# Performance work log

Measured on AMD Instinct MI355X. Metric: run time of the kernel, lower is better.

## Reference

```python
import jax, jax.numpy as jnp
import numpy as np
from jax.ops import segment_sum, segment_max

N, H, E, NEXP, K, L, HEADS, NM = 384, 768, 12288, 8, 2, 3, 4, 38
GAMMA, LAMBDA_SPD = 2.0, 0.5


def _ln(x, g, b, eps=1e-5):
    m = jnp.mean(x, -1, keepdims=True)
    v = jnp.mean((x - m) ** 2, -1, keepdims=True)
    return (x - m) / jnp.sqrt(v + eps) * g + b


def _gelu(x):
    return jax.nn.gelu(x, approximate=False)


def setup_inputs() -> dict:
    key = jax.random.key(0)
    ks = jax.random.split(key, 20)
    r = lambda i, sh: jax.random.normal(ks[i], sh, jnp.float32) * 0.02
    z = lambda sh: jnp.zeros(sh, jnp.float32)
    o = lambda sh: jnp.ones(sh, jnp.float32)
    return dict(
        feat_text=jax.random.normal(ks[0], (N, H), jnp.float32),
        feat_image=jax.random.normal(ks[1], (N, H), jnp.float32),
        spd_matrix=jax.random.uniform(ks[2], (N, N), dtype=jnp.float32),
        src=jax.random.randint(ks[3], (E,), 0, N, jnp.int32),
        dst=jax.random.randint(ks[4], (E,), 0, N, jnp.int32),
        mask_idx=jax.random.randint(ks[5], (NM,), 0, N, jnp.int32),
        mask_token=r(6, (H,)),
        gate_W=r(7, (H, NEXP)), gate_b=z((NEXP,)),
        exp_W1=r(8, (NEXP, H, H)), exp_b1=z((NEXP, H)),
        exp_g1=o((NEXP, H)), exp_be1=z((NEXP, H)),
        exp_W2=r(9, (NEXP, H, H)), exp_b2=z((NEXP, H)),
        gat_W=r(10, (L, H, HEADS * H)), gat_al=r(11, (L, HEADS, H)),
        gat_ar=r(12, (L, HEADS, H)), gat_b=z((L, HEADS * H)),
        dec_W1=r(13, (2, H, H)), dec_b1=z((2, H)),
        dec_g=o((2, H)), dec_be=z((2, H)),
        dec_W2=r(14, (2, H, H)), dec_b2=z((2, H)),
        spd_W1=r(15, (2 * H, H)), spd_b1=z((H,)),
        spd_g=o((H,)), spd_be=z((H,)),
        spd_W2=r(16, (H, 1)), spd_b2=z((1,)),
    )


def _forward(feat_text, feat_image, spd_matrix, mask_token, gate_W, gate_b,
             exp_W1, exp_b1, exp_g1, exp_be1, exp_W2, exp_b2,
             gat_W, gat_al, gat_ar, gat_b,
             dec_W1, dec_b1, dec_g, dec_be, dec_W2, dec_b2,
             spd_W1, spd_b1, spd_g, spd_be, spd_W2, spd_b2,
             src, dst, mask_idx):
    # mean of domain features, then mask-token replacement at fixed indices
    x = (feat_text + feat_image) * 0.5
    xm = x.at[mask_idx].set(mask_token)

    # --- MoE (all experts computed densely, top-2 gathered, as in source) ---
    gw = jax.nn.softmax(xm @ gate_W + gate_b, axis=-1)              # [N,NEXP]
    topw, topi = jax.lax.top_k(gw, K)
    topw = topw / jnp.sum(topw, -1, keepdims=True)
    eh = _gelu(_ln(jnp.einsum('nd,edh->neh', xm, exp_W1) + exp_b1, exp_g1, exp_be1))
    eo = jnp.einsum('neh,ehk->nek', eh, exp_W2) + exp_b2            # [N,NEXP,H]
    sel = jnp.take_along_axis(eo, topi[:, :, None], axis=1)          # [N,K,H]
    h = jnp.sum(sel * topw[:, :, None], axis=1)                      # [N,H]

    # --- stacked GATConv layers (DGL semantics), head-mean after each ---
    for l in range(L):
        f = (h @ gat_W[l]).reshape(N, HEADS, H)                      # [N,heads,H]
        el = jnp.sum(f * gat_al[l], -1)                              # [N,heads]
        er = jnp.sum(f * gat_ar[l], -1)
        e = jax.nn.leaky_relu(el[src] + er[dst], 0.2)                # [E,heads]
        emax = segment_max(e, dst, num_segments=N)
        emax = jnp.where(jnp.isfinite(emax), emax, 0.0)
        ex = jnp.exp(e - emax[dst])
        den = segment_sum(ex, dst, num_segments=N)
        alpha = ex / jnp.maximum(den[dst], 1e-9)                     # edge softmax by dst
        rst = segment_sum(alpha[:, :, None] * f[src], dst, num_segments=N)
        h = jnp.mean(rst + gat_b[l].reshape(HEADS, H), axis=1)       # [N,H]

    # --- domain reconstruction loss on masked nodes ---
    hm = h[mask_idx]
    feats = (feat_text, feat_image)
    recon = jnp.float32(0.0)
    for d in range(2):
        zz = _gelu(_ln(hm @ dec_W1[d] + dec_b1[d], dec_g[d], dec_be[d]))
        rec = zz @ dec_W2[d] + dec_b2[d]
        orig = feats[d][mask_idx]
        denom = jnp.maximum(jnp.linalg.norm(rec, axis=-1) * jnp.linalg.norm(orig, axis=-1), 1e-8)
        cos = jnp.sum(rec * orig, -1) / denom
        recon = recon + jnp.mean((1.0 - cos) ** GAMMA)

    # --- SPD loss over all N^2 pairs, vectorized ---
    # concat([h_i, h_j]) @ W1 == h_i @ W1[:H] + h_j @ W1[H:]  (exact decomposition)
    pa = h @ spd_W1[:H]                                              # [N,H]
    pb = h @ spd_W1[H:]                                              # [N,H]
    zp = _gelu(_ln(pa[:, None, :] + pb[None, :, :] + spd_b1, spd_g, spd_be))  # [N,N,H]
    pred = (zp @ spd_W2)[..., 0] + spd_b2[0]                         # [N,N]
    spd_loss = jnp.mean((pred - spd_matrix) ** 2)

    total = recon + LAMBDA_SPD * spd_loss
    return total, h


def reference(feat_text, feat_image, spd_matrix, src, dst, mask_idx, mask_token,
              gate_W, gate_b, exp_W1, exp_b1, exp_g1, exp_be1, exp_W2, exp_b2,
              gat_W, gat_al, gat_ar, gat_b,
              dec_W1, dec_b1, dec_g, dec_be, dec_W2, dec_b2,
              spd_W1, spd_b1, spd_g, spd_be, spd_W2, spd_b2):
    return _forward(feat_text, feat_image, spd_matrix, mask_token, gate_W, gate_b,
                    exp_W1, exp_b1, exp_g1, exp_be1, exp_W2, exp_b2,
                    gat_W, gat_al, gat_ar, gat_b,
                    dec_W1, dec_b1, dec_g, dec_be, dec_W2, dec_b2,
                    spd_W1, spd_b1, spd_g, spd_be, spd_W2, spd_b2,
                    src, dst, mask_idx)
```

## Files before the change

kernel.cpp:

```cpp
#include <hip/hip_runtime.h>
#include <hip/hip_bf16.h>
#include <math.h>

#define NN 384
#define HD 768
#define EE 12288
#define NCHUNK (EE / 256)
#define NEXPERT 8
#define TOPK 2
#define NLAYER 3
#define NHEADS 4
#define NMASK 38

typedef __attribute__((ext_vector_type(8))) short short8v;
typedef __attribute__((ext_vector_type(4))) float f32x4;
typedef __attribute__((ext_vector_type(2))) float f32x2;
typedef __attribute__((ext_vector_type(4))) int int4v;

__device__ __forceinline__ float gelu_f(float x) {
    return x * 0.5f * (1.f + erff(x * 0.70710678118654752440f));
}

__device__ __forceinline__ ushort f2bf(float x) {
    unsigned u = __float_as_uint(x);
    u += 0x7fffu + ((u >> 16) & 1u);
    return (ushort)(u >> 16);
}

__global__ __launch_bounds__(256) void k_xm_gate_hist(const float* __restrict__ a,
        const float* __restrict__ b, const int* __restrict__ mask_idx,
        const float* __restrict__ mt, ushort* __restrict__ xm_bf,
        const float* __restrict__ gW, const float* __restrict__ gb,
        int* __restrict__ topi, float* __restrict__ topw,
        const int* __restrict__ dst, int* __restrict__ counts) {
    if (blockIdx.x >= NN) {
        __shared__ int h[NN];
        int c = blockIdx.x - NN;
        for (int i = threadIdx.x; i < NN; i += 256) h[i] = 0;
        __syncthreads();
        atomicAdd(&h[dst[c * 256 + threadIdx.x]], 1);
        __syncthreads();
        for (int i = threadIdx.x; i < NN; i += 256) counts[c * NN + i] = h[i];
        return;
    }
    int n = blockIdx.x, tid = threadIdx.x;
    __shared__ float xs[HD];
    __shared__ int ism;
    __shared__ float logits[NEXPERT];
    if (tid == 0) ism = 0;
    __syncthreads();
    if (tid < NMASK && mask_idx[tid] == n) ism = 1;
    __syncthreads();
#pragma unroll
    for (int r = 0; r < 3; r++) {
        int j = r * 256 + tid;
        float v = ism ? mt[j] : 0.5f * (a[(size_t)n * HD + j] + b[(size_t)n * HD + j]);
        xs[j] = v;
        xm_bf[(size_t)n * HD + j] = f2bf(v);
    }
    __syncthreads();
    int grp = tid >> 5;
    int l32 = tid & 31;
    float p = 0.f;
    for (int dd = l32; dd < HD; dd += 32) p += xs[dd] * gW[dd * NEXPERT + grp];
#pragma unroll
    for (int m = 1; m < 32; m <<= 1) p += __shfl_xor(p, m, 32);
    if (l32 == 0) logits[grp] = p + gb[grp];
    __syncthreads();
    if (tid == 0) {
        float mx = logits[0];
#pragma unroll
        for (int e = 1; e < NEXPERT; e++) mx = fmaxf(mx, logits[e]);
        float sm[NEXPERT]; float s = 0.f;
#pragma unroll
        for (int e = 0; e < NEXPERT; e++) { sm[e] = expf(logits[e] - mx); s += sm[e]; }
#pragma unroll
        for (int e = 0; e < NEXPERT; e++) sm[e] /= s;
        int i0 = 0; float b0 = sm[0];
#pragma unroll
        for (int e = 1; e < NEXPERT; e++) if (sm[e] > b0) { b0 = sm[e]; i0 = e; }
        int i1 = -1; float b1v = -1.f;
#pragma unroll
        for (int e = 0; e < NEXPERT; e++) if (e != i0 && sm[e] > b1v) { b1v = sm[e]; i1 = e; }
        float ssum = b0 + b1v;
        topi[n * 2] = i0; topi[n * 2 + 1] = i1;
        topw[n * 2] = b0 / ssum; topw[n * 2 + 1] = b1v / ssum;
    }
}

__global__ __launch_bounds__(256) void k_transpose_all(
        const float* __restrict__ w1, const float* __restrict__ w2,
        const float* __restrict__ gw, const float* __restrict__ sw,
        const float* __restrict__ dw1, const float* __restrict__ dw2,
        ushort* __restrict__ o1, ushort* __restrict__ o2, ushort* __restrict__ og,
        ushort* __restrict__ os, ushort* __restrict__ od1, ushort* __restrict__ od2) {
    int b = blockIdx.x;
    const float* src; ushort* dst; int N, loc, tilesX;
    if (b < 2304)      { src = w1;  dst = o1;  N = HD;     loc = b;        tilesX = 24; }
    else if (b < 4608) { src = w2;  dst = o2;  N = HD;     loc = b - 2304; tilesX = 24; }
    else if (b < 8064) { src = gw;  dst = og;  N = 4 * HD; loc = b - 4608; tilesX = 96; }
    else if (b < 8640) { src = sw;  dst = os;  N = HD;     loc = b - 8064; tilesX = 24; }
    else if (b < 9216) { src = dw1; dst = od1; N = HD;     loc = b - 8640; tilesX = 24; }
    else               { src = dw2; dst = od2; N = HD;     loc = b - 9216; tilesX = 24; }
    const int K = HD;
    int tilesPerZ = tilesX * 12;
    int z = loc / tilesPerZ;
    int rem = loc - z * tilesPerZ;
    int ty = rem / tilesX, tx = rem - ty * tilesX;
    const float* inz = src + (size_t)z * K * N;
    ushort* outz = dst + (size_t)z * K * N;
    int n0 = tx * 32, k0 = ty * 64;

    __shared__ float t[64][33];
    int r = threadIdx.x >> 2, c8 = (threadIdx.x & 3) * 8;
    const float* ip = inz + (size_t)(k0 + r) * N + n0 + c8;
    float4 va = *reinterpret_cast<const float4*>(ip);
    float4 vb = *reinterpret_cast<const float4*>(ip + 4);
    t[r][c8 + 0] = va.x; t[r][c8 + 1] = va.y; t[r][c8 + 2] = va.z; t[r][c8 + 3] = va.w;
    t[r][c8 + 4] = vb.x; t[r][c8 + 5] = vb.y; t[r][c8 + 6] = vb.z; t[r][c8 + 7] = vb.w;
    __syncthreads();
    int nn = threadIdx.x >> 3;
    int kk = (threadIdx.x & 7) * 8;
    uint4 o;
    uint pk[4];
#pragma unroll
    for (int q = 0; q < 4; q++) {
        ushort lo = f2bf(t[kk + 2 * q][nn]);
        ushort hi = f2bf(t[kk + 2 * q + 1][nn]);
        pk[q] = (uint)lo | ((uint)hi << 16);
    }
    o.x = pk[0]; o.y = pk[1]; o.z = pk[2]; o.w = pk[3];
    *reinterpret_cast<uint4*>(outz + (size_t)(n0 + nn) * K + k0 + kk) = o;
}

__global__ __launch_bounds__(NN) void k_scan_meta(const int* __restrict__ counts,
        int* __restrict__ chunkbase, int* __restrict__ nstart,
        const int* __restrict__ topi, int* __restrict__ ecnt, int* __restrict__ estart,
        int* __restrict__ posArr, int* __restrict__ eofpos, int* __restrict__ rowlist,
        int* __restrict__ dec_rs) {
    int tid = threadIdx.x;
    if (blockIdx.x == 0) {
        __shared__ int tot[NN];
        int n = tid;
        int s = 0;
        for (int c = 0; c < NCHUNK; c++) { chunkbase[c * NN + n] = s; s += counts[c * NN + n]; }
        tot[n] = s;
        __syncthreads();
        for (int off = 1; off < NN; off <<= 1) {
            int v = tot[n];
            int add = (n >= off) ? tot[n - off] : 0;
            __syncthreads();
            tot[n] = v + add;
            __syncthreads();
        }
        nstart[n + 1] = tot[n];
        if (n == 0) nstart[0] = 0;
        return;
    }
    __shared__ int ti[NN * TOPK];
    __shared__ int cnt[NEXPERT];
    __shared__ int est[NEXPERT + 1];
    if (tid < NEXPERT) cnt[tid] = 0;
    __syncthreads();
    for (int a = tid; a < NN * TOPK; a += NN) ti[a] = topi[a];
    __syncthreads();
    for (int a = tid; a < NN * TOPK; a += NN) atomicAdd(&cnt[ti[a]], 1);
    __syncthreads();
    if (tid == 0) {
        int s = 0;
        for (int e = 0; e < NEXPERT; e++) { est[e] = s; s += cnt[e]; }
        est[NEXPERT] = s;
        dec_rs[0] = 0; dec_rs[1] = NMASK;
    }
    __syncthreads();
    if (tid < NEXPERT) { ecnt[tid] = cnt[tid]; estart[tid] = est[tid]; }
    if (tid == 0) estart[NEXPERT] = est[NEXPERT];
    for (int a = tid; a < NN * TOPK; a += NN) {
        int e = ti[a]; int rank = 0;
        for (int a2 = 0; a2 < a; a2++) rank += (ti[a2] == e) ? 1 : 0;
        int p = est[e] + rank;
        posArr[a] = p; eofpos[p] = e; rowlist[p] = a >> 1;
    }
}

__global__ __launch_bounds__(256) void k_rank2(const int* __restrict__ dst,
        const int* __restrict__ chunkbase, const int* __restrict__ nstart,
        int* __restrict__ esorted) {
    __shared__ int ds[256];
    int c = blockIdx.x;
    int e = c * 256 + threadIdx.x;
    int d = dst[e];
    ds[threadIdx.x] = d;
    __syncthreads();
    int r = 0;
    for (int i = 0; i < threadIdx.x; i++) r += (ds[i] == d) ? 1 : 0;
    esorted[nstart[d] + chunkbase[c * NN + d] + r] = e;
}

__device__ __forceinline__ short8v ldfrag(const ushort* s, int r, int kb) {
    int c = kb ^ (r & 7);
    return *reinterpret_cast<const short8v*>(s + r * 64 + c * 8);
}

__device__ __forceinline__ void gemm_body(
        const ushort* __restrict__ A, const ushort* __restrict__ Bt, float* __restrict__ C,
        int M, int Ncol, int K, int lda, int ldc, long strideBt, long strideC,
        const int* __restrict__ rowsA, const int* __restrict__ Ms,
        const int* __restrict__ rowStarts, int z, ushort* Asm, ushort* Bsm) {
    int Meff = Ms ? Ms[z] : M;
    int row0 = blockIdx.y * 64;
    if (row0 >= Meff) return;
    int col0 = blockIdx.x * 64;
    if (col0 >= Ncol) return;
    int rowbase = rowStarts ? rowStarts[z] : 0;
    const ushort* Btz = Bt + (size_t)z * strideBt;
    float* Cz = C + (size_t)rowbase * ldc + (size_t)z * strideC;
    const int* rz = rowsA ? (rowsA + rowbase) : nullptr;

    int tid = threadIdx.x;
    int w = tid >> 6, lane = tid & 63;
    int wr = w >> 1, wc = w & 1;
    int l15 = lane & 15, lq = lane >> 4;

    int r0s = tid >> 3, c0s = tid & 7;
    int cs0 = c0s ^ (r0s & 7);
    int r1s = r0s + 32;
    int cs1 = c0s ^ (r1s & 7);
    int grow0 = row0 + r0s, grow1 = row0 + r1s;
    bool ok0 = grow0 < Meff, ok1 = grow1 < Meff;
    int srow0 = ok0 ? (rz ? rz[grow0] : rowbase + grow0) : (rz ? rz[0] : rowbase);
    int srow1 = ok1 ? (rz ? rz[grow1] : rowbase + grow1) : (rz ? rz[0] : rowbase);
    const ushort* aP0 = A + (size_t)srow0 * lda + c0s * 8;
    const ushort* aP1 = A + (size_t)srow1 * lda + c0s * 8;
    const ushort* bP0 = Btz + (size_t)(col0 + r0s) * K + c0s * 8;
    const ushort* bP1 = Btz + (size_t)(col0 + r1s) * K + c0s * 8;
    ushort* asm0 = &Asm[r0s * 64 + cs0 * 8];
    ushort* asm1 = &Asm[r1s * 64 + cs1 * 8];
    ushort* bsm0 = &Bsm[r0s * 64 + cs0 * 8];
    ushort* bsm1 = &Bsm[r1s * 64 + cs1 * 8];
    const int4v z4 = (int4v){0, 0, 0, 0};

    f32x4 acc[2][2];
#pragma unroll
    for (int i = 0; i < 2; i++)
#pragma unroll
        for (int j = 0; j < 2; j++) acc[i][j] = (f32x4){0.f, 0.f, 0.f, 0.f};

    int4v ta0 = *reinterpret_cast<const int4v*>(aP0);
    int4v ta1 = *reinterpret_cast<const int4v*>(aP1);
    int4v av0 = ok0 ? ta0 : z4;
    int4v av1 = ok1 ? ta1 : z4;
    int4v bv0 = *reinterpret_cast<const int4v*>(bP0);
    int4v bv1 = *reinterpret_cast<const int4v*>(bP1);

    for (int k0 = 0; k0 < K; k0 += 64) {
        *reinterpret_cast<int4v*>(asm0) = av0;
        *reinterpret_cast<int4v*>(asm1) = av1;
        *reinterpret_cast<int4v*>(bsm0) = bv0;
        *reinterpret_cast<int4v*>(bsm1) = bv1;
        __syncthreads();
        int kn = k0 + 64;
        if (kn < K) {
            int4v na0 = *reinterpret_cast<const int4v*>(aP0 + kn);
            int4v na1 = *reinterpret_cast<const int4v*>(aP1 + kn);
            av0 = ok0 ? na0 : z4;
            av1 = ok1 ? na1 : z4;
            bv0 = *reinterpret_cast<const int4v*>(bP0 + kn);
            bv1 = *reinterpret_cast<const int4v*>(bP1 + kn);
        }
#pragma unroll
        for (int ks = 0; ks < 2; ks++) {
            int kb = ks * 4 + lq;
            short8v a0 = ldfrag(Asm, wr * 32 + l15, kb);
            short8v a1 = ldfrag(Asm, wr * 32 + 16 + l15, kb);
            short8v b0 = ldfrag(Bsm, wc * 32 + l15, kb);
            short8v b1 = ldfrag(Bsm, wc * 32 + 16 + l15, kb);
            acc[0][0] = __builtin_amdgcn_mfma_f32_16x16x32_bf16(a0, b0, acc[0][0], 0, 0, 0);
            acc[0][1] = __builtin_amdgcn_mfma_f32_16x16x32_bf16(a0, b1, acc[0][1], 0, 0, 0);
            acc[1][0] = __builtin_amdgcn_mfma_f32_16x16x32_bf16(a1, b0, acc[1][0], 0, 0, 0);
            acc[1][1] = __builtin_amdgcn_mfma_f32_16x16x32_bf16(a1, b1, acc[1][1], 0, 0, 0);
        }
        __syncthreads();
    }
#pragma unroll
    for (int ai = 0; ai < 2; ai++)
#pragma unroll
        for (int bi = 0; bi < 2; bi++) {
            int rbase = row0 + wr * 32 + ai * 16 + (lq << 2);
            int cc = col0 + wc * 32 + bi * 16 + l15;
#pragma unroll
            for (int r = 0; r < 4; r++) {
                int rr = rbase + r;
                if (rr < Meff) Cz[(size_t)rr * ldc + cc] = acc[ai][bi][r];
            }
        }
}

__global__ __launch_bounds__(256) void k_mfma_gemm(
        const ushort* __restrict__ A, const ushort* __restrict__ Bt, float* __restrict__ C,
        int M, int Ncol, int K, int lda, int ldc, long strideBt, long strideC,
        const int* __restrict__ rowsA, const int* __restrict__ Ms,
        const int* __restrict__ rowStarts) {
    __shared__ ushort Asm[64 * 64];
    __shared__ ushort Bsm[64 * 64];
    gemm_body(A, Bt, C, M, Ncol, K, lda, ldc, strideBt, strideC, rowsA, Ms, rowStarts,
              blockIdx.z, Asm, Bsm);
}

__global__ __launch_bounds__(256) void k_mfma_dual(
        const ushort* __restrict__ A0, const ushort* __restrict__ Bt0, float* __restrict__ C0,
        int M0, int Nc0, int lda0, int ldc0, long sBt0, long sC0,
        const int* __restrict__ rows0, const int* __restrict__ rs0, int nz0,
        const ushort* __restrict__ A1, const ushort* __restrict__ Bt1, float* __restrict__ C1,
        int M1, int Nc1, int lda1, int ldc1, long sBt1, long sC1,
        const int* __restrict__ rows1, const int* __restrict__ rs1) {
    __shared__ ushort Asm[64 * 64];
    __shared__ ushort Bsm[64 * 64];
    int z = blockIdx.z;
    if (z < nz0)
        gemm_body(A0, Bt0, C0, M0, Nc0, HD, lda0, ldc0, sBt0, sC0, rows0, nullptr, rs0,
                  z, Asm, Bsm);
    else
        gemm_body(A1, Bt1, C1, M1, Nc1, HD, lda1, ldc1, sBt1, sC1, rows1, nullptr, rs1,
                  z - nz0, Asm, Bsm);
}

__global__ __launch_bounds__(256) void k_ln_gelu(const float* __restrict__ t1,
        ushort* __restrict__ ehb, const float* __restrict__ b1, const float* __restrict__ g,
        const float* __restrict__ be, const int* __restrict__ eofpos) {
    int row = blockIdx.x;
    int e = eofpos[row];
    int tid = threadIdx.x;
    __shared__ float rA[4], rB[4];
    float v[3]; float s1 = 0.f, s2 = 0.f;
#pragma unroll
    for (int r = 0; r < 3; r++) {
        int c = r * 256 + tid;
        float x = t1[(size_t)row * HD + c] + b1[e * HD + c];
        v[r] = x; s1 += x; s2 += x * x;
    }
#pragma unroll
    for (int m = 1; m < 64; m <<= 1) { s1 += __shfl_xor(s1, m); s2 += __shfl_xor(s2, m); }
    int wave = tid >> 6, lane = tid & 63;
    if (lane == 0) { rA[wave] = s1; rB[wave] = s2; }
    __syncthreads();
    float S1 = rA[0] + rA[1] + rA[2] + rA[3];
    float S2 = rB[0] + rB[1] + rB[2] + rB[3];
    float mean = S1 * (1.f / HD);
    float var = S2 * (1.f / HD) - mean * mean;
    float rstd = rsqrtf(var + 1e-5f);
#pragma unroll
    for (int r = 0; r < 3; r++) {
        int c = r * 256 + tid;
        float zn = (v[r] - mean) * rstd * g[e * HD + c] + be[e * HD + c];
        ehb[(size_t)row * HD + c] = f2bf(gelu_f(zn));
    }
}

__global__ void k_combine_moe(const float* __restrict__ eo, const float* __restrict__ b2,
        const int* __restrict__ topi, const float* __restrict__ topw,
        const int* __restrict__ posArr, float* __restrict__ h, ushort* __restrict__ hb) {
    int n = blockIdx.x;
    int tid = threadIdx.x;
    int e0 = topi[n * 2], e1 = topi[n * 2 + 1];
    float w0 = topw[n * 2], w1 = topw[n * 2 + 1];
    int p0 = posArr[n * 2], p1 = posArr[n * 2 + 1];
    for (int j = tid; j < HD; j += 256) {
        float v0 = eo[(size_t)p0 * HD + j] + b2[e0 * HD + j];
        float v1 = eo[(size_t)p1 * HD + j] + b2[e1 * HD + j];
        float hv = w0 * v0 + w1 * v1;
        h[(size_t)n * HD + j] = hv;
        hb[(size_t)n * HD + j] = f2bf(hv);
    }
}

__global__ __launch_bounds__(256) void k_el_er(const float* __restrict__ f,
        const float* __restrict__ al, const float* __restrict__ ar,
        float* __restrict__ el, float* __restrict__ er) {
    int n = blockIdx.x;
    int hd = threadIdx.x >> 6, lane = threadIdx.x & 63;
    const float* fr = f + ((size_t)n * NHEADS + hd) * HD;
    float pl = 0.f, pr = 0.f;
    for (int j = lane; j < HD; j += 64) {
        float fv = fr[j];
        pl += fv * al[hd * HD + j];
        pr += fv * ar[hd * HD + j];
    }
#pragma unroll
    for (int m = 1; m < 64; m <<= 1) { pl += __shfl_xor(pl, m); pr += __shfl_xor(pr, m); }
    if (lane == 0) { el[n * NHEADS + hd] = pl; er[n * NHEADS + hd] = pr; }
}

__global__ __launch_bounds__(256) void k_gat_agg(const float* __restrict__ f,
        const float* __restrict__ el, const float* __restrict__ er,
        const int* __restrict__ src, const int* __restrict__ esorted,
        const int* __restrict__ nstart, const float* __restrict__ gb,
        float* __restrict__ hout, ushort* __restrict__ hb, float* __restrict__ outp) {
    int n = blockIdx.x;
    int s0 = nstart[n], cnt = nstart[n + 1] - s0;
    int tid = threadIdx.x;
    __shared__ float red[4][NHEADS];
    __shared__ float emax_s[NHEADS], den_s[NHEADS];
    __shared__ float alpha_s[256][NHEADS];
    __shared__ int sn_s[256];
    float ern[NHEADS];
#pragma unroll
    for (int hd = 0; hd < NHEADS; hd++) ern[hd] = er[n * NHEADS + hd];
    int wave = tid >> 6, lane = tid & 63;

    float mx[NHEADS] = { -1e30f, -1e30f, -1e30f, -1e30f };
    for (int t = tid; t < cnt; t += 256) {
        int e = esorted[s0 + t]; int sn = src[e];
#pragma unroll
        for (int hd = 0; hd < NHEADS; hd++) {
            float v = el[sn * NHEADS + hd] + ern[hd];
            v = (v >= 0.f) ? v : 0.2f * v;
            mx[hd] = fmaxf(mx[hd], v);
        }
    }
#pragma unroll
    for (int hd = 0; hd < NHEADS; hd++) {
#pragma unroll
        for (int m = 1; m < 64; m <<= 1) mx[hd] = fmaxf(mx[hd], __shfl_xor(mx[hd], m));
    }
    if (lane == 0) { for (int hd = 0; hd < NHEADS; hd++) red[wave][hd] = mx[hd]; }
    __syncthreads();
    if (tid == 0) {
#pragma unroll
        for (int hd = 0; hd < NHEADS; hd++)
            emax_s[hd] = fmaxf(fmaxf(red[0][hd], red[1][hd]), fmaxf(red[2][hd], red[3][hd]));
    }
    __syncthreads();
    float sm[NHEADS] = { 0.f, 0.f, 0.f, 0.f };
    for (int t = tid; t < cnt; t += 256) {
        int e = esorted[s0 + t]; int sn = src[e];
#pragma unroll
        for (int hd = 0; hd < NHEADS; hd++) {
            float v = el[sn * NHEADS + hd] + ern[hd];
            v = (v >= 0.f) ? v : 0.2f * v;
            sm[hd] += expf(v - emax_s[hd]);
        }
    }
#pragma unroll
    for (int hd = 0; hd < NHEADS; hd++) {
#pragma unroll
        for (int m = 1; m < 64; m <<= 1) sm[hd] += __shfl_xor(sm[hd], m);
    }
    __syncthreads();
    if (lane == 0) { for (int hd = 0; hd < NHEADS; hd++) red[wave][hd] = sm[hd]; }
    __syncthreads();
    if (tid == 0) {
#pragma unroll
        for (int hd = 0; hd < NHEADS; hd++)
            den_s[hd] = red[0][hd] + red[1][hd] + red[2][hd] + red[3][hd];
    }
    __syncthreads();
    float acc[NHEADS][3] = {};
    for (int c0 = 0; c0 < cnt; c0 += 256) {
        int t = c0 + tid;
        if (t < cnt) {
            int e = esorted[s0 + t]; int sn = src[e];
            sn_s[tid] = sn;
#pragma unroll
            for (int hd = 0; hd < NHEADS; hd++) {
                float v = el[sn * NHEADS + hd] + ern[hd];
                v = (v >= 0.f) ? v : 0.2f * v;
                alpha_s[tid][hd] = expf(v - emax_s[hd]) / fmaxf(den_s[hd], 1e-9f);
            }
        }
        __syncthreads();
        int cm = cnt - c0; if (cm > 256) cm = 256;
        for (int i = 0; i < cm; i++) {
            int sn = sn_s[i];
            const float* fr = f + (size_t)sn * (NHEADS * HD);
#pragma unroll
            for (int hd = 0; hd < NHEADS; hd++) {
                float a = alpha_s[i][hd];
#pragma unroll
                for (int r = 0; r < 3; r++) acc[hd][r] += a * fr[hd * HD + r * 256 + tid];
            }
        }
        __syncthreads();
    }
#pragma unroll
    for (int r = 0; r < 3; r++) {
        int j = r * 256 + tid;
        float s = 0.f;
#pragma unroll
        for (int hd = 0; hd < NHEADS; hd++) s += acc[hd][r] + gb[hd * HD + j];
        float hv = 0.25f * s;
        hout[(size_t)n * HD + j] = hv;
        hb[(size_t)n * HD + j] = f2bf(hv);
        if (outp) outp[1 + (size_t)n * HD + j] = hv;
    }
}

__global__ __launch_bounds__(256) void k_lndec_prep(float* __restrict__ pab,
        const float* __restrict__ b1, ushort* __restrict__ pp_bf,
        float* __restrict__ Svec, float* __restrict__ Qvec,
        const float* __restrict__ t1, ushort* __restrict__ zzb,
        const float* __restrict__ db1, const float* __restrict__ dg,
        const float* __restrict__ dbe) {
    int tid = threadIdx.x;
    int wave = tid >> 6, lane = tid & 63;
    __shared__ float rA[4], rB[4];
    if (blockIdx.x >= 2 * NN) {
        int row = blockIdx.x - 2 * NN;
        int d = row / NMASK;
        float v[3]; float s1 = 0.f, s2 = 0.f;
#pragma unroll
        for (int r = 0; r < 3; r++) {
            int c = r * 256 + tid;
            float x = t1[(size_t)row * HD + c] + db1[d * HD + c];
            v[r] = x; s1 += x; s2 += x * x;
        }
#pragma unroll
        for (int mm = 1; mm < 64; mm <<= 1) { s1 += __shfl_xor(s1, mm); s2 += __shfl_xor(s2, mm); }
        if (lane == 0) { rA[wave] = s1; rB[wave] = s2; }
        __syncthreads();
        float S1 = rA[0] + rA[1] + rA[2] + rA[3];
        float S2 = rB[0] + rB[1] + rB[2] + rB[3];
        float mean = S1 * (1.f / HD);
        float var = S2 * (1.f / HD) - mean * mean;
        float rstd = rsqrtf(var + 1e-5f);
#pragma unroll
        for (int r = 0; r < 3; r++) {
            int c = r * 256 + tid;
            float zn = (v[r] - mean) * rstd * dg[d * HD + c] + dbe[d * HD + c];
            zzb[(size_t)row * HD + c] = f2bf(gelu_f(zn));
        }
        return;
    }
    int r = blockIdx.x;
    bool isA = r < NN;
    float* row = pab + (size_t)r * HD;
    float vv[3]; float s1 = 0.f, s2 = 0.f;
#pragma unroll
    for (int rr = 0; rr < 3; rr++) {
        int j = rr * 256 + tid;
        float v = row[j];
        if (isA) v += b1[j];
        vv[rr] = v; s1 += v; s2 += v * v;
    }
#pragma unroll
    for (int m = 1; m < 64; m <<= 1) { s1 += __shfl_xor(s1, m); s2 += __shfl_xor(s2, m); }
    if (lane == 0) { rA[wave] = s1; rB[wave] = s2; }
#pragma unroll
    for (int rr = 0; rr < 3; rr++) {
        int j = rr * 256 + tid;
        if (isA) row[j] = vv[rr];
        pp_bf[(size_t)r * HD + j] = f2bf(vv[rr]);
    }
    __syncthreads();
    if (tid == 0) {
        Svec[r] = rA[0] + rA[1] + rA[2] + rA[3];
        Qvec[r] = rB[0] + rB[1] + rB[2] + rB[3];
    }
}

#define GC1 2.3022085f
#define GC2 0.10294429f
__global__ __launch_bounds__(256) void k_spd2(const float* __restrict__ pab,
        const float* __restrict__ Svec, const float* __restrict__ Qvec,
        const float* __restrict__ cross, const float* __restrict__ g,
        const float* __restrict__ be, const float* __restrict__ w2,
        const float* __restrict__ b2, const float* __restrict__ spd,
        float* __restrict__ partials,
        const float* __restrict__ rec, const float* __restrict__ db2,
        const int* __restrict__ mask_idx, const float* __restrict__ ft,
        const float* __restrict__ fi, float* __restrict__ rec_part) {
    int wv = threadIdx.x >> 6, lane = threadIdx.x & 63;
    if (blockIdx.y == 8) {
        int b = blockIdx.x;
        if (b >= 2 * NMASK) return;
        int d = b / NMASK, m = b % NMASK;
        int node = mask_idx[m];
        int tid = threadIdx.x;
        __shared__ float rA[4], rB[4], rC[4];
        const float* rrow = rec + (size_t)b * HD;
        const float* orig = (d == 0 ? ft : fi) + (size_t)node * HD;
        float pro = 0.f, prr = 0.f, poo = 0.f;
#pragma unroll
        for (int r = 0; r < 3; r++) {
            int c = r * 256 + tid;
            float rv = rrow[c] + db2[d * HD + c];
            float o = orig[c];
            pro += rv * o; prr += rv * rv; poo += o * o;
        }
#pragma unroll
        for (int mm = 1; mm < 64; mm <<= 1) {
            pro += __shfl_xor(pro, mm); prr += __shfl_xor(prr, mm); poo += __shfl_xor(poo, mm);
        }
        if (lane == 0) { rA[wv] = pro; rB[wv] = prr; rC[wv] = poo; }
        __syncthreads();
        if (tid == 0) {
            float P = rA[0] + rA[1] + rA[2] + rA[3];
            float R = rB[0] + rB[1] + rB[2] + rB[3];
            float O = rC[0] + rC[1] + rC[2] + rC[3];
            float denom = fmaxf(sqrtf(R) * sqrtf(O), 1e-8f);
            float cosv = P / denom;
            float t = 1.f - cosv;
            rec_part[b] = (t * t) * (1.f / (float)NMASK);
        }
        return;
    }
    int i = blockIdx.x;
    int y = blockIdx.y * 4 + wv;
    const f32x2* paP = reinterpret_cast<const f32x2*>(pab + (size_t)i * HD) + lane;
    const f32x2* gP  = reinterpret_cast<const f32x2*>(g) + lane;
    const f32x2* beP = reinterpret_cast<const f32x2*>(be) + lane;
    const f32x2* wP  = reinterpret_cast<const f32x2*>(w2) + lane;
    f32x2 pa2[6], g2[6], be2[6], w22[6];
#pragma unroll
    for (int s = 0; s < 6; s++) {
        pa2[s] = paP[s * 64];
        g2[s]  = gP[s * 64];
        be2[s] = beP[s * 64];
        w22[s] = wP[s * 64];
    }
#pragma unroll
    for (int s = 0; s < 6; s++) {
        asm volatile("" : "+v"(pa2[s]), "+v"(g2[s]), "+v"(be2[s]), "+v"(w22[s]));
    }
    const f32x2 C1v = (f32x2){GC1, GC1};
    const f32x2 C2v = (f32x2){GC2, GC2};
    const f32x2 one2 = (f32x2){1.f, 1.f};
    float Sa = Svec[i], Qa = Qvec[i];
    float b2v = b2[0];
    float bacc = 0.f;
#pragma unroll
    for (int t = 0; t < 6; t++) {
        int ja = y + (2 * t) * 32;
        int jb = y + (2 * t + 1) * 32;
        const f32x2* pA = reinterpret_cast<const f32x2*>(pab + (size_t)(NN + ja) * HD) + lane;
        const f32x2* pB = reinterpret_cast<const f32x2*>(pab + (size_t)(NN + jb) * HD) + lane;
        float meanA = (Sa + Svec[NN + ja]) * (1.f / HD);
        float exA = (Qa + Qvec[NN + ja] + 2.f * cross[(size_t)i * NN + ja]) * (1.f / HD);
        float rsA = rsqrtf(exA - meanA * meanA + 1e-5f);
        float nmA = -meanA * rsA;
        float meanB = (Sa + Svec[NN + jb]) * (1.f / HD);
        float exB = (Qa + Qvec[NN + jb] + 2.f * cross[(size_t)i * NN + jb]) * (1.f / HD);
        float rsB = rsqrtf(exB - meanB * meanB + 1e-5f);
        float nmB = -meanB * rsB;
        f32x2 rsA2 = (f32x2){rsA, rsA}, nmA2 = (f32x2){nmA, nmA};
        f32x2 rsB2 = (f32x2){rsB, rsB}, nmB2 = (f32x2){nmB, nmB};
        f32x2 dA = (f32x2){0.f, 0.f}, dB = (f32x2){0.f, 0.f};
#pragma unroll
        for (int s = 0; s < 6; s++) {
            f32x2 zA = pa2[s] + pA[s * 64];
            f32x2 zB = pa2[s] + pB[s * 64];
            f32x2 znA = (zA * rsA2 + nmA2) * g2[s] + be2[s];
            f32x2 znB = (zB * rsB2 + nmB2) * g2[s] + be2[s];
            f32x2 uaA = znA * (znA * znA * C2v + C1v);
            f32x2 uaB = znB * (znB * znB * C2v + C1v);
            f32x2 eA, eB;
            eA.x = __builtin_amdgcn_exp2f(-uaA.x);
            eA.y = __builtin_amdgcn_exp2f(-uaA.y);
            eB.x = __builtin_amdgcn_exp2f(-uaB.x);
            eB.y = __builtin_amdgcn_exp2f(-uaB.y);
            f32x2 qA = eA + one2;
            f32x2 qB = eB + one2;
            f32x2 rrA, rrB;
            rrA.x = __builtin_amdgcn_rcpf(qA.x);
            rrA.y = __builtin_amdgcn_rcpf(qA.y);
            rrB.x = __builtin_amdgcn_rcpf(qB.x);
            rrB.y = __builtin_amdgcn_rcpf(qB.y);
            f32x2 nwA = znA * w22[s];
            f32x2 nwB = znB * w22[s];
            dA = nwA * rrA + dA;
            dB = nwB * rrB + dB;
        }
        float dotA = dA.x + dA.y;
        float dotB = dB.x + dB.y;
#pragma unroll
        for (int m = 1; m < 64; m <<= 1) {
            dotA += __shfl_xor(dotA, m);
            dotB += __shfl_xor(dotB, m);
        }
        if (lane == 0) {
            float da = (dotA + b2v) - spd[(size_t)i * NN + ja];
            float db = (dotB + b2v) - spd[(size_t)i * NN + jb];
            bacc += da * da + db * db;
        }
    }
    if (lane == 0) partials[i * 32 + y] = bacc;
}

__global__ __launch_bounds__(256) void k_out(const float* __restrict__ rec_part,
        const float* __restrict__ spd_part, float* __restrict__ out) {
    __shared__ float rA[4], rB[4];
    int tid = threadIdx.x;
    float sp = 0.f, rc = 0.f;
    for (int t = tid; t < 32 * NN; t += 256) sp += spd_part[t];
    for (int t = tid; t < 2 * NMASK; t += 256) rc += rec_part[t];
#pragma unroll
    for (int m = 1; m < 64; m <<= 1) { sp += __shfl_xor(sp, m); rc += __shfl_xor(rc, m); }
    int wave = tid >> 6, lane = tid & 63;
    if (lane == 0) { rA[wave] = sp; rB[wave] = rc; }
    __syncthreads();
    if (tid == 0) {
        float SP = rA[0] + rA[1] + rA[2] + rA[3];
        float RC = rB[0] + rB[1] + rB[2] + rB[3];
        out[0] = RC + 0.5f * (SP * (1.f / ((float)NN * (float)NN)));
    }
}

extern "C" void kernel_launch(void* const* d_in, const int* in_sizes, int n_in,
                              void* d_out, int out_size, void* d_ws, size_t ws_size,
                              hipStream_t stream) {
    const float* feat_text = (const float*)d_in[0];
    const float* feat_image = (const float*)d_in[1];
    const float* spd_matrix = (const float*)d_in[2];
    const int*   src       = (const int*)d_in[3];
    const int*   dst       = (const int*)d_in[4];
    const int*   mask_idx  = (const int*)d_in[5];
    const float* mask_token = (const float*)d_in[6];
    const float* gate_W = (const float*)d_in[7];
    const float* gate_b = (const float*)d_in[8];
    const float* exp_W1 = (const float*)d_in[9];
    const float* exp_b1 = (const float*)d_in[10];
    const float* exp_g1 = (const float*)d_in[11];
    const float* exp_be1 = (const float*)d_in[12];
    const float* exp_W2 = (const float*)d_in[13];
    const float* exp_b2 = (const float*)d_in[14];
    const float* gat_W  = (const float*)d_in[15];
    const float* gat_al = (const float*)d_in[16];
    const float* gat_ar = (const float*)d_in[17];
    const float* gat_b  = (const float*)d_in[18];
    const float* dec_W1 = (const float*)d_in[19];
    const float* dec_b1 = (const float*)d_in[20];
    const float* dec_g  = (const float*)d_in[21];
    const float* dec_be = (const float*)d_in[22];
    const float* dec_W2 = (const float*)d_in[23];
    const float* dec_b2 = (const float*)d_in[24];
    const float* spd_W1 = (const float*)d_in[25];
    const float* spd_b1 = (const float*)d_in[26];
    const float* spd_g  = (const float*)d_in[27];
    const float* spd_be = (const float*)d_in[28];
    const float* spd_W2 = (const float*)d_in[29];
    const float* spd_b2 = (const float*)d_in[30];
    (void)in_sizes; (void)n_in; (void)ws_size; (void)out_size;

    float* ws = (float*)d_ws;
    size_t off = 0;
    auto alloc = [&](size_t nfl) { float* p = ws + off; off += (nfl + 3) & ~(size_t)3; return p; };
    float* hA   = alloc((size_t)NN * HD);
    float* hB   = alloc((size_t)NN * HD);
    float* t1   = alloc((size_t)NN * TOPK * HD);
    float* eo   = alloc((size_t)NN * TOPK * HD);
    float* fbuf = alloc((size_t)NN * NHEADS * HD);
    float* el   = alloc(NN * NHEADS);
    float* er   = alloc(NN * NHEADS);
    float* pab  = alloc((size_t)2 * NN * HD);
    float* cross = alloc((size_t)NN * NN);
    float* Svec = alloc(2 * NN);
    float* Qvec = alloc(2 * NN);
    float* topw = alloc(NN * TOPK);
    float* rec_part = alloc(2 * NMASK + 4);
    float* spd_part = alloc(32 * NN);
    int* topi    = (int*)alloc(NN * TOPK);
    int* ecnt    = (int*)alloc(16);
    int* estart  = (int*)alloc(16);
    int* posArr  = (int*)alloc(NN * TOPK);
    int* eofpos  = (int*)alloc(NN * TOPK);
    int* rowlist = (int*)alloc(NN * TOPK);
    int* dec_rs  = (int*)alloc(4);
    int* nstart  = (int*)alloc(NN + 4);
    int* esorted = (int*)alloc(EE);
    int* counts    = (int*)alloc((size_t)NCHUNK * NN);
    int* chunkbase = (int*)alloc((size_t)NCHUNK * NN);
    ushort* xm_bf  = (ushort*)alloc((size_t)NN * HD / 2);
    ushort* eh_bf  = (ushort*)alloc((size_t)NN * TOPK * HD / 2);
    ushort* hA_bf  = (ushort*)alloc((size_t)NN * HD / 2);
    ushort* hB_bf  = (ushort*)alloc((size_t)NN * HD / 2);
    ushort* pp_bf  = (ushort*)alloc((size_t)2 * NN * HD / 2);
    ushort* expW1t = (ushort*)alloc((size_t)NEXPERT * HD * HD / 2);
    ushort* expW2t = (ushort*)alloc((size_t)NEXPERT * HD * HD / 2);
    ushort* gatWt  = (ushort*)alloc((size_t)NLAYER * NHEADS * HD * HD / 2);
    ushort* spdW1t = (ushort*)alloc((size_t)2 * HD * HD / 2);
    ushort* decW1t = (ushort*)alloc((size_t)2 * HD * HD / 2);
    ushort* decW2t = (ushort*)alloc((size_t)2 * HD * HD / 2);

    k_transpose_all<<<dim3(9792), dim3(256), 0, stream>>>(
        exp_W1, exp_W2, gat_W, spd_W1, dec_W1, dec_W2,
        expW1t, expW2t, gatWt, spdW1t, decW1t, decW2t);

    k_xm_gate_hist<<<dim3(NN + NCHUNK), dim3(256), 0, stream>>>(
        feat_text, feat_image, mask_idx, mask_token, xm_bf, gate_W, gate_b, topi, topw,
        dst, counts);

    k_scan_meta<<<dim3(2), dim3(NN), 0, stream>>>(
        counts, chunkbase, nstart, topi, ecnt, estart, posArr, eofpos, rowlist, dec_rs);
    k_rank2<<<dim3(NCHUNK), dim3(256), 0, stream>>>(dst, chunkbase, nstart, esorted);

    k_mfma_gemm<<<dim3(HD / 64, 12, NEXPERT), dim3(256), 0, stream>>>(
        xm_bf, expW1t, t1, 0, HD, HD, HD, HD, (long)HD * HD, 0, rowlist, ecnt, estart);
    k_ln_gelu<<<dim3(NN * TOPK), dim3(256), 0, stream>>>(t1, eh_bf, exp_b1, exp_g1, exp_be1, eofpos);
    k_mfma_gemm<<<dim3(HD / 64, 12, NEXPERT), dim3(256), 0, stream>>>(
        eh_bf, expW2t, eo, 0, HD, HD, HD, HD, (long)HD * HD, 0, nullptr, ecnt, estart);
    k_combine_moe<<<dim3(NN), dim3(256), 0, stream>>>(eo, exp_b2, topi, topw, posArr, hA, hA_bf);

    float* hcur = hA; float* hnxt = hB;
    ushort* hcur_bf = hA_bf; ushort* hnxt_bf = hB_bf;
    for (int l = 0; l < NLAYER; l++) {
        k_mfma_gemm<<<dim3(NHEADS * HD / 64, NN / 64, 1), dim3(256), 0, stream>>>(
            hcur_bf, gatWt + (size_t)l * NHEADS * HD * HD, fbuf,
            NN, NHEADS * HD, HD, HD, NHEADS * HD, 0, 0, nullptr, nullptr, nullptr);
        k_el_er<<<dim3(NN), dim3(256), 0, stream>>>(
            fbuf, gat_al + (size_t)l * NHEADS * HD, gat_ar + (size_t)l * NHEADS * HD, el, er);
        k_gat_agg<<<dim3(NN), dim3(256), 0, stream>>>(
            fbuf, el, er, src, esorted, nstart, gat_b + (size_t)l * NHEADS * HD, hnxt, hnxt_bf,
            (l == NLAYER - 1) ? (float*)d_out : nullptr);
        float* t = hcur; hcur = hnxt; hnxt = t;
        ushort* tb = hcur_bf; hcur_bf = hnxt_bf; hnxt_bf = tb;
    }
    ushort* hfin_bf = hcur_bf;

    k_mfma_dual<<<dim3(HD / 64, NN / 64, 4), dim3(256), 0, stream>>>(
        hfin_bf, spdW1t, pab, NN, HD, HD, HD, (long)HD * HD, (long)NN * HD,
        nullptr, nullptr, 2,
        hfin_bf, decW1t, t1, NMASK, HD, HD, HD, (long)HD * HD, (long)NMASK * HD,
        mask_idx, nullptr);

    k_lndec_prep<<<dim3(2 * NN + 2 * NMASK), dim3(256), 0, stream>>>(
        pab, spd_b1, pp_bf, Svec, Qvec, t1, eh_bf, dec_b1, dec_g, dec_be);

    k_mfma_dual<<<dim3(HD / 64, NN / 64, 3), dim3(256), 0, stream>>>(
        eh_bf, decW2t, eo, NMASK, HD, HD, HD, (long)HD * HD, 0,
        nullptr, dec_rs, 2,
        pp_bf, pp_bf + (size_t)NN * HD, cross, NN, NN, HD, NN, 0, 0,
        nullptr, nullptr);

    k_spd2<<<dim3(NN, 9), dim3(256), 0, stream>>>(
        pab, Svec, Qvec, cross, spd_g, spd_be, spd_W2, spd_b2, spd_matrix, spd_part,
        eo, dec_b2, mask_idx, feat_text, feat_image, rec_part);

    k_out<<<dim3(1), dim3(256), 0, stream>>>(rec_part, spd_part, (float*)d_out);
}
```

Measured before the change: 296.0 us.

## Fold GAT attention vectors into projection weights as extra GEMM columns

Precomputes W·a_l and W·a_r for each head and layer, stores them as 8 extra output columns of the transposed GAT weight, and widens the GEMM N dimension to 3136. This removes the separate el/er reduction kernel, which re-read the full projected features each layer. The aggregation kernel now reads el/er straight from the widened feature rows. The cost is a slightly larger GEMM, an extra precompute block set in the transpose kernel, and el/er computed from bf16-rounded folded weights, which can shift values slightly.

```diff
diff --git a/kernel.cpp b/kernel.cpp
--- a/kernel.cpp
+++ b/kernel.cpp
@@ -11,6 +11,7 @@
 #define NLAYER 3
 #define NHEADS 4
 #define NMASK 38
+#define GATB 3136
 
 typedef __attribute__((ext_vector_type(8))) short short8v;
 typedef __attribute__((ext_vector_type(4))) float f32x4;
@@ -93,34 +94,73 @@
         const float* __restrict__ gw, const float* __restrict__ sw,
         const float* __restrict__ dw1, const float* __restrict__ dw2,
         ushort* __restrict__ o1, ushort* __restrict__ o2, ushort* __restrict__ og,
-        ushort* __restrict__ os, ushort* __restrict__ od1, ushort* __restrict__ od2) {
+        ushort* __restrict__ os, ushort* __restrict__ od1, ushort* __restrict__ od2,
+        const float* __restrict__ gal, const float* __restrict__ gar) {
+    __shared__ float smem[8448];
     int b = blockIdx.x;
-    const float* src; ushort* dst; int N, loc, tilesX;
-    if (b < 2304)      { src = w1;  dst = o1;  N = HD;     loc = b;        tilesX = 24; }
-    else if (b < 4608) { src = w2;  dst = o2;  N = HD;     loc = b - 2304; tilesX = 24; }
-    else if (b < 8064) { src = gw;  dst = og;  N = 4 * HD; loc = b - 4608; tilesX = 96; }
-    else if (b < 8640) { src = sw;  dst = os;  N = HD;     loc = b - 8064; tilesX = 24; }
-    else if (b < 9216) { src = dw1; dst = od1; N = HD;     loc = b - 8640; tilesX = 24; }
-    else               { src = dw2; dst = od2; N = HD;     loc = b - 9216; tilesX = 24; }
+    int tid = threadIdx.x;
+    if (b >= 9792) {
+        int b2 = b - 9792;
+        int l = b2 / 12, kc = b2 % 12;
+        float* aLDS = smem;
+        float* red = smem + 6144;
+        for (int idx = tid; idx < 8 * HD; idx += 256) {
+            int ri = idx / HD, j = idx - ri * HD;
+            aLDS[idx] = (ri < 4) ? gal[((size_t)l * 4 + ri) * HD + j]
+                                 : gar[((size_t)l * 4 + (ri - 4)) * HD + j];
+        }
+        __syncthreads();
+        int q = tid >> 6, kk = tid & 63;
+        int k = kc * 64 + kk;
+        const float* wrow = gw + ((size_t)l * HD + k) * (4 * HD);
+        float acc[8] = {};
+        for (int j = q * 192; j < q * 192 + 192; j++) {
+            float w0 = wrow[0 * HD + j], w1v = wrow[1 * HD + j];
+            float w2v = wrow[2 * HD + j], w3 = wrow[3 * HD + j];
+            acc[0] += w0 * aLDS[0 * HD + j]; acc[4] += w0 * aLDS[4 * HD + j];
+            acc[1] += w1v * aLDS[1 * HD + j]; acc[5] += w1v * aLDS[5 * HD + j];
+            acc[2] += w2v * aLDS[2 * HD + j]; acc[6] += w2v * aLDS[6 * HD + j];
+            acc[3] += w3 * aLDS[3 * HD + j]; acc[7] += w3 * aLDS[7 * HD + j];
+        }
+#pragma unroll
+        for (int ri = 0; ri < 8; ri++) red[(q * 64 + kk) * 8 + ri] = acc[ri];
+        __syncthreads();
+        if (tid < 64) {
+#pragma unroll
+            for (int ri = 0; ri < 8; ri++) {
+                float s = red[(0 * 64 + tid) * 8 + ri] + red[(1 * 64 + tid) * 8 + ri]
+                        + red[(2 * 64 + tid) * 8 + ri] + red[(3 * 64 + tid) * 8 + ri];
+                og[(size_t)l * GATB * HD + (size_t)(3072 + ri) * HD + kc * 64 + tid] = f2bf(s);
+            }
+        }
+        return;
+    }
+    const float* src; ushort* dst; int N, loc, tilesX; size_t outStrideZ;
+    if (b < 2304)      { src = w1;  dst = o1;  N = HD;     loc = b;        tilesX = 24; outStrideZ = (size_t)HD * HD; }
+    else if (b < 4608) { src = w2;  dst = o2;  N = HD;     loc = b - 2304; tilesX = 24; outStrideZ = (size_t)HD * HD; }
+    else if (b < 8064) { src = gw;  dst = og;  N = 4 * HD; loc = b - 4608; tilesX = 96; outStrideZ = (size_t)GATB * HD; }
+    else if (b < 8640) { src = sw;  dst = os;  N = HD;     loc = b - 8064; tilesX = 24; outStrideZ = (size_t)HD * HD; }
+    else if (b < 9216) { src = dw1; dst = od1; N = HD;     loc = b - 8640; tilesX = 24; outStrideZ = (size_t)HD * HD; }
+    else               { src = dw2; dst = od2; N = HD;     loc = b - 9216; tilesX = 24; outStrideZ = (size_t)HD * HD; }
     const int K = HD;
     int tilesPerZ = tilesX * 12;
     int z = loc / tilesPerZ;
     int rem = loc - z * tilesPerZ;
     int ty = rem / tilesX, tx = rem - ty * tilesX;
     const float* inz = src + (size_t)z * K * N;
-    ushort* outz = dst + (size_t)z * K * N;
+    ushort* outz = dst + (size_t)z * outStrideZ;
     int n0 = tx * 32, k0 = ty * 64;
 
-    __shared__ float t[64][33];
-    int r = threadIdx.x >> 2, c8 = (threadIdx.x & 3) * 8;
+    float (*t)[33] = reinterpret_cast<float (*)[33]>(smem);
+    int r = tid >> 2, c8 = (tid & 3) * 8;
     const float* ip = inz + (size_t)(k0 + r) * N + n0 + c8;
     float4 va = *reinterpret_cast<const float4*>(ip);
     float4 vb = *reinterpret_cast<const float4*>(ip + 4);
     t[r][c8 + 0] = va.x; t[r][c8 + 1] = va.y; t[r][c8 + 2] = va.z; t[r][c8 + 3] = va.w;
     t[r][c8 + 4] = vb.x; t[r][c8 + 5] = vb.y; t[r][c8 + 6] = vb.z; t[r][c8 + 7] = vb.w;
     __syncthreads();
-    int nn = threadIdx.x >> 3;
-    int kk = (threadIdx.x & 7) * 8;
+    int nn = tid >> 3;
+    int kk = (tid & 7) * 8;
     uint4 o;
     uint pk[4];
 #pragma unroll
@@ -374,25 +414,7 @@
     }
 }
 
-__global__ __launch_bounds__(256) void k_el_er(const float* __restrict__ f,
-        const float* __restrict__ al, const float* __restrict__ ar,
-        float* __restrict__ el, float* __restrict__ er) {
-    int n = blockIdx.x;
-    int hd = threadIdx.x >> 6, lane = threadIdx.x & 63;
-    const float* fr = f + ((size_t)n * NHEADS + hd) * HD;
-    float pl = 0.f, pr = 0.f;
-    for (int j = lane; j < HD; j += 64) {
-        float fv = fr[j];
-        pl += fv * al[hd * HD + j];
-        pr += fv * ar[hd * HD + j];
-    }
-#pragma unroll
-    for (int m = 1; m < 64; m <<= 1) { pl += __shfl_xor(pl, m); pr += __shfl_xor(pr, m); }
-    if (lane == 0) { el[n * NHEADS + hd] = pl; er[n * NHEADS + hd] = pr; }
-}
-
 __global__ __launch_bounds__(256) void k_gat_agg(const float* __restrict__ f,
-        const float* __restrict__ el, const float* __restrict__ er,
         const int* __restrict__ src, const int* __restrict__ esorted,
         const int* __restrict__ nstart, const float* __restrict__ gb,
         float* __restrict__ hout, ushort* __restrict__ hb, float* __restrict__ outp) {
@@ -403,17 +425,18 @@
     __shared__ float emax_s[NHEADS], den_s[NHEADS];
     __shared__ float alpha_s[256][NHEADS];
     __shared__ int sn_s[256];
-    float ern[NHEADS];
-#pragma unroll
-    for (int hd = 0; hd < NHEADS; hd++) ern[hd] = er[n * NHEADS + hd];
+    float4 ernv = *reinterpret_cast<const float4*>(f + (size_t)n * GATB + 3076);
+    float ern[NHEADS] = { ernv.x, ernv.y, ernv.z, ernv.w };
     int wave = tid >> 6, lane = tid & 63;
 
     float mx[NHEADS] = { -1e30f, -1e30f, -1e30f, -1e30f };
     for (int t = tid; t < cnt; t += 256) {
         int e = esorted[s0 + t]; int sn = src[e];
+        float4 elv = *reinterpret_cast<const float4*>(f + (size_t)sn * GATB + 3072);
+        float el4[NHEADS] = { elv.x, elv.y, elv.z, elv.w };
 #pragma unroll
         for (int hd = 0; hd < NHEADS; hd++) {
-            float v = el[sn * NHEADS + hd] + ern[hd];
+            float v = el4[hd] + ern[hd];
             v = (v >= 0.f) ? v : 0.2f * v;
             mx[hd] = fmaxf(mx[hd], v);
         }
@@ -434,9 +457,11 @@
     float sm[NHEADS] = { 0.f, 0.f, 0.f, 0.f };
     for (int t = tid; t < cnt; t += 256) {
         int e = esorted[s0 + t]; int sn = src[e];
+        float4 elv = *reinterpret_cast<const float4*>(f + (size_t)sn * GATB + 3072);
+        float el4[NHEADS] = { elv.x, elv.y, elv.z, elv.w };
 #pragma unroll
         for (int hd = 0; hd < NHEADS; hd++) {
-            float v = el[sn * NHEADS + hd] + ern[hd];
+            float v = el4[hd] + ern[hd];
             v = (v >= 0.f) ? v : 0.2f * v;
             sm[hd] += expf(v - emax_s[hd]);
         }
@@ -461,9 +486,11 @@
         if (t < cnt) {
             int e = esorted[s0 + t]; int sn = src[e];
             sn_s[tid] = sn;
+            float4 elv = *reinterpret_cast<const float4*>(f + (size_t)sn * GATB + 3072);
+            float el4[NHEADS] = { elv.x, elv.y, elv.z, elv.w };
 #pragma unroll
             for (int hd = 0; hd < NHEADS; hd++) {
-                float v = el[sn * NHEADS + hd] + ern[hd];
+                float v = el4[hd] + ern[hd];
                 v = (v >= 0.f) ? v : 0.2f * v;
                 alpha_s[tid][hd] = expf(v - emax_s[hd]) / fmaxf(den_s[hd], 1e-9f);
             }
@@ -472,7 +499,7 @@
         int cm = cnt - c0; if (cm > 256) cm = 256;
         for (int i = 0; i < cm; i++) {
             int sn = sn_s[i];
-            const float* fr = f + (size_t)sn * (NHEADS * HD);
+            const float* fr = f + (size_t)sn * GATB;
 #pragma unroll
             for (int hd = 0; hd < NHEADS; hd++) {
                 float a = alpha_s[i][hd];
@@ -748,9 +775,7 @@
     float* hB   = alloc((size_t)NN * HD);
     float* t1   = alloc((size_t)NN * TOPK * HD);
     float* eo   = alloc((size_t)NN * TOPK * HD);
-    float* fbuf = alloc((size_t)NN * NHEADS * HD);
-    float* el   = alloc(NN * NHEADS);
-    float* er   = alloc(NN * NHEADS);
+    float* fbuf = alloc((size_t)NN * GATB);
     float* pab  = alloc((size_t)2 * NN * HD);
     float* cross = alloc((size_t)NN * NN);
     float* Svec = alloc(2 * NN);
@@ -776,14 +801,14 @@
     ushort* pp_bf  = (ushort*)alloc((size_t)2 * NN * HD / 2);
     ushort* expW1t = (ushort*)alloc((size_t)NEXPERT * HD * HD / 2);
     ushort* expW2t = (ushort*)alloc((size_t)NEXPERT * HD * HD / 2);
-    ushort* gatWt  = (ushort*)alloc((size_t)NLAYER * NHEADS * HD * HD / 2);
+    ushort* gatWt  = (ushort*)alloc((size_t)NLAYER * GATB * HD / 2);
     ushort* spdW1t = (ushort*)alloc((size_t)2 * HD * HD / 2);
     ushort* decW1t = (ushort*)alloc((size_t)2 * HD * HD / 2);
     ushort* decW2t = (ushort*)alloc((size_t)2 * HD * HD / 2);
 
-    k_transpose_all<<<dim3(9792), dim3(256), 0, stream>>>(
+    k_transpose_all<<<dim3(9792 + 36), dim3(256), 0, stream>>>(
         exp_W1, exp_W2, gat_W, spd_W1, dec_W1, dec_W2,
-        expW1t, expW2t, gatWt, spdW1t, decW1t, decW2t);
+        expW1t, expW2t, gatWt, spdW1t, decW1t, decW2t, gat_al, gat_ar);
 
     k_xm_gate_hist<<<dim3(NN + NCHUNK), dim3(256), 0, stream>>>(
         feat_text, feat_image, mask_idx, mask_token, xm_bf, gate_W, gate_b, topi, topw,
@@ -803,13 +828,11 @@
     float* hcur = hA; float* hnxt = hB;
     ushort* hcur_bf = hA_bf; ushort* hnxt_bf = hB_bf;
     for (int l = 0; l < NLAYER; l++) {
-        k_mfma_gemm<<<dim3(NHEADS * HD / 64, NN / 64, 1), dim3(256), 0, stream>>>(
-            hcur_bf, gatWt + (size_t)l * NHEADS * HD * HD, fbuf,
-            NN, NHEADS * HD, HD, HD, NHEADS * HD, 0, 0, nullptr, nullptr, nullptr);
-        k_el_er<<<dim3(NN), dim3(256), 0, stream>>>(
-            fbuf, gat_al + (size_t)l * NHEADS * HD, gat_ar + (size_t)l * NHEADS * HD, el, er);
+        k_mfma_gemm<<<dim3(GATB / 64, NN / 64, 1), dim3(256), 0, stream>>>(
+            hcur_bf, gatWt + (size_t)l * GATB * HD, fbuf,
+            NN, GATB, HD, HD, GATB, 0, 0, nullptr, nullptr, nullptr);
         k_gat_agg<<<dim3(NN), dim3(256), 0, stream>>>(
-            fbuf, el, er, src, esorted, nstart, gat_b + (size_t)l * NHEADS * HD, hnxt, hnxt_bf,
+            fbuf, src, esorted, nstart, gat_b + (size_t)l * NHEADS * HD, hnxt, hnxt_bf,
             (l == NLAYER - 1) ? (float*)d_out : nullptr);
         float* t = hcur; hcur = hnxt; hnxt = t;
         ushort* tb = hcur_bf; hcur_bf = hnxt_bf; hnxt_bf = tb;
```

Measured after the change: 314.0 us. 6.1% more time.
